# Kernel optimization log

Hardware: AMD Instinct MI355X
Metric: run time of the kernel (lower is better)

## Reference

```python
import jax, jax.numpy as jnp
import numpy as np

B, S, Lb, C, CP, H = 64, 4, 64, 32, 16, 4
LN_EPS = 1e-5


def layer_norm(x, g, b):
    mu = jnp.mean(x, axis=-1, keepdims=True)
    var = jnp.mean(jnp.square(x - mu), axis=-1, keepdims=True)
    return (x - mu) * jax.lax.rsqrt(var + LN_EPS) * g + b


def mha(x, w_in, b_in, w_out, b_out, h):
    # torch nn.MultiheadAttention, batch_first, self-attention
    Bx, L, Cx = x.shape
    d = Cx // h
    qkv = x @ w_in.T + b_in                      # (Bx, L, 3C)
    q, k, v = jnp.split(qkv, 3, axis=-1)
    sp = lambda t: t.reshape(Bx, L, h, d).transpose(0, 2, 1, 3)  # (Bx,h,L,d)
    q, k, v = sp(q), sp(k), sp(v)
    scale = 1.0 / jnp.sqrt(jnp.asarray(d, x.dtype))
    attn = jax.nn.softmax(jnp.einsum('bhid,bhjd->bhij', q, k) * scale, axis=-1)
    o = jnp.einsum('bhij,bhjd->bhid', attn, v).transpose(0, 2, 1, 3).reshape(Bx, L, Cx)
    return o @ w_out.T + b_out


def setup_inputs() -> dict:
    key = jax.random.key(0)
    ks = jax.random.split(key, 20)
    g = lambda i, shape, s=0.05: (jax.random.normal(ks[i], shape, dtype=jnp.float32) * s)
    inp = {
        'chip_ctcf': jax.random.normal(ks[0], (B, Lb), dtype=jnp.float32),
        'chip_hac':  jax.random.normal(ks[1], (B, Lb), dtype=jnp.float32),
        'chip_me1':  jax.random.normal(ks[2], (B, Lb), dtype=jnp.float32),
        'chip_me3':  jax.random.normal(ks[3], (B, Lb), dtype=jnp.float32),
        'embed_w': g(4, (C, 1)), 'embed_b': g(5, (C,)),
        'pos_embed': g(6, (1, 1, Lb, C), 0.02),
        'row_in_w': g(7, (3 * C, C)), 'row_in_b': g(8, (3 * C,)),
        'row_out_w': g(9, (C, C)), 'row_out_b': g(10, (C,)),
        'row_ln_g': jnp.ones((C,), jnp.float32), 'row_ln_b': jnp.zeros((C,), jnp.float32),
        'col_in_w': g(11, (3 * C, C)), 'col_in_b': g(12, (3 * C,)),
        'col_out_w': g(13, (C, C)), 'col_out_b': g(14, (C,)),
        'col_ln_g': jnp.ones((C,), jnp.float32), 'col_ln_b': jnp.zeros((C,), jnp.float32),
        'proj_w': g(15, (CP, C * C)), 'proj_b': g(16, (CP,)),
        'pln_g': jnp.ones((CP,), jnp.float32), 'pln_b': jnp.zeros((CP,), jnp.float32),
    }
    return inp


def reference(chip_ctcf, chip_hac, chip_me1, chip_me3,
              embed_w, embed_b, pos_embed,
              row_in_w, row_in_b, row_out_w, row_out_b, row_ln_g, row_ln_b,
              col_in_w, col_in_b, col_out_w, col_out_b, col_ln_g, col_ln_b,
              proj_w, proj_b, pln_g, pln_b):
    Bv = chip_ctcf.shape[0]
    signals = jnp.stack([chip_ctcf, chip_hac, chip_me1, chip_me3], axis=1)  # (B,4,64)
    # Linear(1, C): scalar embed
    msa = signals[..., None] * embed_w[:, 0] + embed_b                      # (B,4,64,C)
    msa = msa + pos_embed
    # row attention over the 64 bins, per track
    x = msa.reshape(Bv * S, Lb, C)
    x = layer_norm(x + mha(x, row_in_w, row_in_b, row_out_w, row_out_b, H), row_ln_g, row_ln_b)
    msa = x.reshape(Bv, S, Lb, C)
    # column attention over the 4 tracks, per bin
    x = msa.transpose(0, 2, 1, 3).reshape(Bv * Lb, S, C)
    x = layer_norm(x + mha(x, col_in_w, col_in_b, col_out_w, col_out_b, H), col_ln_g, col_ln_b)
    msa = x.reshape(Bv, Lb, S, C).transpose(0, 2, 1, 3)                     # (B,4,64,C)
    # outer product of the track-mean (as written in the torch source)
    m = jnp.mean(msa, axis=1)                                               # (B,64,C)
    pair = jnp.einsum('bic,bjd->bijcd', m, m).reshape(Bv, Lb, Lb, C * C)    # (B,64,64,1024)
    nrm = jnp.sqrt(jnp.sum(jnp.square(pair), axis=-1, keepdims=True))
    pair = pair / jnp.maximum(nrm, 1e-6)                                    # F.normalize eps=1e-6
    feat = pair @ proj_w.T + proj_b                                         # (B,64,64,CP)
    feat = layer_norm(feat, pln_g, pln_b)
    feat = feat * jax.nn.sigmoid(feat)                                      # SiLU
    return feat.transpose(0, 3, 1, 2)                                       # (B,CP,64,64)
```

## Files before the change

kernel.cpp:

```cpp
#include <hip/hip_runtime.h>
#include <hip/hip_bf16.h>

#define LN_EPS 1e-5f

__device__ __forceinline__ float dot8(float4 a0, float4 a1, float4 b0, float4 b1) {
    return a0.x * b0.x + a0.y * b0.y + a0.z * b0.z + a0.w * b0.w +
           a1.x * b1.x + a1.y * b1.y + a1.z * b1.z + a1.w * b1.w;
}

__global__ __launch_bounds__(256) void k_row(
    const float* __restrict__ ctcf, const float* __restrict__ hac,
    const float* __restrict__ me1,  const float* __restrict__ me3,
    const float* __restrict__ ew,   const float* __restrict__ eb,
    const float* __restrict__ pe,
    const float* __restrict__ w_in, const float* __restrict__ b_in,
    const float* __restrict__ w_out,const float* __restrict__ b_out,
    const float* __restrict__ ln_g, const float* __restrict__ ln_b,
    float* __restrict__ msaR)
{
    __shared__ float sx[64][33];
    __shared__ float sqkv[64 * 100];
    __shared__ float so[64][33];
    __shared__ float smean[64], srstd[64];

    const int blk = blockIdx.x;
    const int s   = blk & 3;
    const int b   = blk >> 2;
    const int tid = threadIdx.x;

    const float* chip = (s == 0) ? ctcf : (s == 1) ? hac : (s == 2) ? me1 : me3;

    for (int n = tid; n < 2048; n += 256) {
        int l = n >> 5, c = n & 31;
        sx[l][c] = chip[b * 64 + l] * ew[c] + eb[c] + pe[l * 32 + c];
    }
    __syncthreads();

    const int l  = tid & 63;
    const int cg = tid >> 6;

    float xr[32];
#pragma unroll
    for (int c = 0; c < 32; ++c) xr[c] = sx[l][c];

#pragma unroll
    for (int i = 0; i < 24; ++i) {
        int cc = i * 4 + cg;
        const float4* wr4 = (const float4*)&w_in[cc * 32];
        float acc = b_in[cc];
#pragma unroll
        for (int c4 = 0; c4 < 8; ++c4) {
            float4 wv = wr4[c4];
            acc += xr[c4 * 4 + 0] * wv.x + xr[c4 * 4 + 1] * wv.y +
                   xr[c4 * 4 + 2] * wv.z + xr[c4 * 4 + 3] * wv.w;
        }
        sqkv[l * 100 + cc] = acc;
    }
    __syncthreads();

    {
        const int h = cg;
        const float4* qp = (const float4*)&sqkv[l * 100 + h * 8];
        float4 q0 = qp[0], q1 = qp[1];
        const float scale = 0.35355339059327373f;
        float mrun = -1e30f, denom = 0.f, a[8];
#pragma unroll
        for (int dd = 0; dd < 8; ++dd) a[dd] = 0.f;
        for (int j = 0; j < 64; ++j) {
            const float4* kp = (const float4*)&sqkv[j * 100 + 32 + h * 8];
            float4 k0 = kp[0], k1 = kp[1];
            float sc = dot8(q0, q1, k0, k1) * scale;
            const float4* vp = (const float4*)&sqkv[j * 100 + 64 + h * 8];
            float4 v0 = vp[0], v1 = vp[1];
            float mnew = fmaxf(mrun, sc);
            float corr = __expf(mrun - mnew);
            float w = __expf(sc - mnew);
            denom = denom * corr + w;
            a[0] = a[0] * corr + w * v0.x;  a[1] = a[1] * corr + w * v0.y;
            a[2] = a[2] * corr + w * v0.z;  a[3] = a[3] * corr + w * v0.w;
            a[4] = a[4] * corr + w * v1.x;  a[5] = a[5] * corr + w * v1.y;
            a[6] = a[6] * corr + w * v1.z;  a[7] = a[7] * corr + w * v1.w;
            mrun = mnew;
        }
        float inv = 1.f / denom;
#pragma unroll
        for (int dd = 0; dd < 8; ++dd) so[l][h * 8 + dd] = a[dd] * inv;
    }
    __syncthreads();

    {
        float orow[32];
#pragma unroll
        for (int k = 0; k < 32; ++k) orow[k] = so[l][k];
#pragma unroll
        for (int i = 0; i < 8; ++i) {
            int c = i * 4 + cg;
            const float4* wr4 = (const float4*)&w_out[c * 32];
            float acc = b_out[c] + xr[c];
#pragma unroll
            for (int k4 = 0; k4 < 8; ++k4) {
                float4 wv = wr4[k4];
                acc += orow[k4 * 4 + 0] * wv.x + orow[k4 * 4 + 1] * wv.y +
                       orow[k4 * 4 + 2] * wv.z + orow[k4 * 4 + 3] * wv.w;
            }
            sqkv[l * 100 + c] = acc;
        }
    }
    __syncthreads();

    if (tid < 64) {
        float mu = 0.f;
#pragma unroll
        for (int c = 0; c < 32; ++c) mu += sqkv[tid * 100 + c];
        mu *= (1.f / 32.f);
        float var = 0.f;
#pragma unroll
        for (int c = 0; c < 32; ++c) { float d = sqkv[tid * 100 + c] - mu; var += d * d; }
        var *= (1.f / 32.f);
        smean[tid] = mu;
        srstd[tid] = rsqrtf(var + LN_EPS);
    }
    __syncthreads();

    float* outp = msaR + blk * 2048;
    for (int n = tid; n < 2048; n += 256) {
        int ll = n >> 5, c = n & 31;
        outp[n] = (sqkv[ll * 100 + c] - smean[ll]) * srstd[ll] * ln_g[c] + ln_b[c];
    }
}

__global__ __launch_bounds__(256) void k_col(
    const float* __restrict__ msaR,
    const float* __restrict__ w_in, const float* __restrict__ b_in,
    const float* __restrict__ w_out,const float* __restrict__ b_out,
    const float* __restrict__ ln_g, const float* __restrict__ ln_b,
    float* __restrict__ m_out, float* __restrict__ nrm_out)
{
    __shared__ float sx[64][33];
    __shared__ float sqkv[64 * 100];
    __shared__ float so[64][33];
    __shared__ float smean2[64], srstd2[64];
    __shared__ float smv[16][33];

    const int bx = blockIdx.x;
    const int b  = bx >> 2;
    const int l0 = (bx & 3) * 16;
    const int tid = threadIdx.x;

    for (int n = tid; n < 2048; n += 256) {
        int s = n >> 9, lo = (n >> 5) & 15, c = n & 31;
        sx[s * 16 + lo][c] = msaR[((b * 4 + s) * 64 + l0 + lo) * 32 + c];
    }
    __syncthreads();

    const int r  = tid & 63;
    const int sS = r & 3, lo = r >> 2;
    const int cg = tid >> 6;

    float xr[32];
#pragma unroll
    for (int c = 0; c < 32; ++c) xr[c] = sx[sS * 16 + lo][c];

#pragma unroll
    for (int i = 0; i < 24; ++i) {
        int cc = i * 4 + cg;
        const float4* wr4 = (const float4*)&w_in[cc * 32];
        float acc = b_in[cc];
#pragma unroll
        for (int c4 = 0; c4 < 8; ++c4) {
            float4 wv = wr4[c4];
            acc += xr[c4 * 4 + 0] * wv.x + xr[c4 * 4 + 1] * wv.y +
                   xr[c4 * 4 + 2] * wv.z + xr[c4 * 4 + 3] * wv.w;
        }
        sqkv[r * 100 + cc] = acc;
    }
    __syncthreads();

    {
        const int la = tid >> 4, h = (tid >> 2) & 3, ia = tid & 3;
        const float scale = 0.35355339059327373f;
        const float4* qp = (const float4*)&sqkv[(la * 4 + ia) * 100 + h * 8];
        float4 q0 = qp[0], q1 = qp[1];
        float sc[4];
        float mx = -1e30f;
#pragma unroll
        for (int jj = 0; jj < 4; ++jj) {
            const float4* kp = (const float4*)&sqkv[(la * 4 + jj) * 100 + 32 + h * 8];
            sc[jj] = dot8(q0, q1, kp[0], kp[1]) * scale;
            mx = fmaxf(mx, sc[jj]);
        }
        float den = 0.f;
#pragma unroll
        for (int jj = 0; jj < 4; ++jj) { sc[jj] = __expf(sc[jj] - mx); den += sc[jj]; }
        float inv = 1.f / den;
        float a[8];
#pragma unroll
        for (int dd = 0; dd < 8; ++dd) a[dd] = 0.f;
#pragma unroll
        for (int jj = 0; jj < 4; ++jj) {
            const float4* vp = (const float4*)&sqkv[(la * 4 + jj) * 100 + 64 + h * 8];
            float4 v0 = vp[0], v1 = vp[1];
            float wgt = sc[jj];
            a[0] += wgt * v0.x;  a[1] += wgt * v0.y;
            a[2] += wgt * v0.z;  a[3] += wgt * v0.w;
            a[4] += wgt * v1.x;  a[5] += wgt * v1.y;
            a[6] += wgt * v1.z;  a[7] += wgt * v1.w;
        }
#pragma unroll
        for (int dd = 0; dd < 8; ++dd) so[la * 4 + ia][h * 8 + dd] = a[dd] * inv;
    }
    __syncthreads();

    {
        float orow[32];
#pragma unroll
        for (int k = 0; k < 32; ++k) orow[k] = so[r][k];
#pragma unroll
        for (int i = 0; i < 8; ++i) {
            int c = i * 4 + cg;
            const float4* wr4 = (const float4*)&w_out[c * 32];
            float acc = b_out[c] + xr[c];
#pragma unroll
            for (int k4 = 0; k4 < 8; ++k4) {
                float4 wv = wr4[k4];
                acc += orow[k4 * 4 + 0] * wv.x + orow[k4 * 4 + 1] * wv.y +
                       orow[k4 * 4 + 2] * wv.z + orow[k4 * 4 + 3] * wv.w;
            }
            sqkv[r * 100 + c] = acc;
        }
    }
    __syncthreads();

    if (tid < 64) {
        float mu = 0.f;
#pragma unroll
        for (int c = 0; c < 32; ++c) mu += sqkv[tid * 100 + c];
        mu *= (1.f / 32.f);
        float var = 0.f;
#pragma unroll
        for (int c = 0; c < 32; ++c) { float d = sqkv[tid * 100 + c] - mu; var += d * d; }
        var *= (1.f / 32.f);
        smean2[tid] = mu;
        srstd2[tid] = rsqrtf(var + LN_EPS);
    }
    __syncthreads();

    for (int pass = 0; pass < 2; ++pass) {
        int idx = pass * 256 + tid;
        int loo = idx >> 5, c = idx & 31;
        float acc = 0.f;
#pragma unroll
        for (int ss = 0; ss < 4; ++ss) {
            int rr = loo * 4 + ss;
            acc += (sqkv[rr * 100 + c] - smean2[rr]) * srstd2[rr];
        }
        float mval = 0.25f * acc * ln_g[c] + ln_b[c];
        m_out[(b * 64 + l0 + loo) * 32 + c] = mval;
        smv[loo][c] = mval * mval;
    }
    __syncthreads();

    if (tid < 16) {
        float sum = 0.f;
#pragma unroll
        for (int c = 0; c < 32; ++c) sum += smv[tid][c];
        nrm_out[b * 64 + l0 + tid] = sqrtf(sum);
    }
}

__global__ __launch_bounds__(256) void k_pair(
    const float* __restrict__ m, const float* __restrict__ nrm,
    const float* __restrict__ pw, const float* __restrict__ pb,
    const float* __restrict__ pg, const float* __restrict__ pbeta,
    float* __restrict__ out)
{
    __shared__ float smj[64][36];
    __shared__ float sT[8 * 520];
    __shared__ float snj[64];
    __shared__ float sbias[16], sgam[16], sbet[16];

    const int bx = blockIdx.x;
    const int b  = bx >> 3;
    const int i0 = (bx & 7) * 8;
    const int tid = threadIdx.x;
    const int lane = tid & 63, w = tid >> 6;

    const int rem0 = lane + 128 * w;
    const int rem1 = rem0 + 64;
    const float* pw0 = pw + (rem0 >> 5) * 1024 + (rem0 & 31);
    const float* pw1 = pw + (rem1 >> 5) * 1024 + (rem1 & 31);
    float w0[32], w1[32];
#pragma unroll
    for (int c = 0; c < 32; ++c) { w0[c] = pw0[c * 32]; w1[c] = pw1[c * 32]; }

    const float* mb = m + b * 2048;
    for (int n = tid; n < 2048; n += 256) smj[n >> 5][n & 31] = mb[n];
    if (tid < 64) snj[tid] = nrm[b * 64 + tid];
    if (tid < 16) {
        sbias[tid] = pb[tid];
        sgam[tid]  = pg[tid];
        sbet[tid]  = pbeta[tid];
    }
    __syncthreads();

#pragma unroll
    for (int il = 0; il < 8; ++il) {
        const float4* mr4 = (const float4*)&smj[i0 + il][0];
        float a0 = 0.f, a1 = 0.f;
#pragma unroll
        for (int c4 = 0; c4 < 8; ++c4) {
            float4 mv = mr4[c4];
            a0 += mv.x * w0[c4 * 4 + 0] + mv.y * w0[c4 * 4 + 1] +
                  mv.z * w0[c4 * 4 + 2] + mv.w * w0[c4 * 4 + 3];
            a1 += mv.x * w1[c4 * 4 + 0] + mv.y * w1[c4 * 4 + 1] +
                  mv.z * w1[c4 * 4 + 2] + mv.w * w1[c4 * 4 + 3];
        }
        sT[il * 520 + rem0] = a0;
        sT[il * 520 + rem1] = a1;
    }
    __syncthreads();

    const int j = lane;
    float mj[32];
    {
        const float4* mjp = (const float4*)&smj[j][0];
#pragma unroll
        for (int d4 = 0; d4 < 8; ++d4) {
            float4 t = mjp[d4];
            mj[d4 * 4 + 0] = t.x;  mj[d4 * 4 + 1] = t.y;
            mj[d4 * 4 + 2] = t.z;  mj[d4 * 4 + 3] = t.w;
        }
    }
    const float nj = snj[j];

#pragma unroll
    for (int q = 0; q < 2; ++q) {
        const int il = w * 2 + q;
        const int ig = i0 + il;
        const float invn = 1.f / fmaxf(snj[ig] * nj, 1e-6f);
        float f[16];
#pragma unroll
        for (int cp = 0; cp < 16; ++cp) {
            const float4* tr = (const float4*)&sT[il * 520 + cp * 32];
            float acc = 0.f;
#pragma unroll
            for (int d4 = 0; d4 < 8; ++d4) {
                float4 tv = tr[d4];
                acc += tv.x * mj[d4 * 4 + 0] + tv.y * mj[d4 * 4 + 1] +
                       tv.z * mj[d4 * 4 + 2] + tv.w * mj[d4 * 4 + 3];
            }
            f[cp] = acc * invn + sbias[cp];
        }
        float mu = 0.f;
#pragma unroll
        for (int cp = 0; cp < 16; ++cp) mu += f[cp];
        mu *= (1.f / 16.f);
        float var = 0.f;
#pragma unroll
        for (int cp = 0; cp < 16; ++cp) { float d = f[cp] - mu; var += d * d; }
        var *= (1.f / 16.f);
        const float rstd = rsqrtf(var + LN_EPS);
#pragma unroll
        for (int cp = 0; cp < 16; ++cp) {
            float v = (f[cp] - mu) * rstd * sgam[cp] + sbet[cp];
            float sl = v / (1.f + __expf(-v));
            out[((b * 16 + cp) * 64 + ig) * 64 + j] = sl;
        }
    }
}

extern "C" void kernel_launch(void* const* d_in, const int* in_sizes, int n_in,
                              void* d_out, int out_size, void* d_ws, size_t ws_size,
                              hipStream_t stream) {
    const float* ctcf  = (const float*)d_in[0];
    const float* hac   = (const float*)d_in[1];
    const float* me1   = (const float*)d_in[2];
    const float* me3   = (const float*)d_in[3];
    const float* ew    = (const float*)d_in[4];
    const float* ebias = (const float*)d_in[5];
    const float* pe    = (const float*)d_in[6];
    const float* riw   = (const float*)d_in[7];
    const float* rib   = (const float*)d_in[8];
    const float* row_  = (const float*)d_in[9];
    const float* rob   = (const float*)d_in[10];
    const float* rlg   = (const float*)d_in[11];
    const float* rlb   = (const float*)d_in[12];
    const float* ciw   = (const float*)d_in[13];
    const float* cib   = (const float*)d_in[14];
    const float* cow   = (const float*)d_in[15];
    const float* cob   = (const float*)d_in[16];
    const float* clg   = (const float*)d_in[17];
    const float* clb   = (const float*)d_in[18];
    const float* pw    = (const float*)d_in[19];
    const float* pb    = (const float*)d_in[20];
    const float* pg    = (const float*)d_in[21];
    const float* pbt   = (const float*)d_in[22];

    float* out = (float*)d_out;

    float* msaR = (float*)d_out;
    float* mbuf = (float*)d_ws;
    float* nbuf = mbuf + 64 * 64 * 32;

    k_row<<<256, 256, 0, stream>>>(ctcf, hac, me1, me3, ew, ebias, pe,
                                   riw, rib, row_, rob, rlg, rlb, msaR);
    k_col<<<256, 256, 0, stream>>>(msaR, ciw, cib, cow, cob, clg, clb,
                                   mbuf, nbuf);
    k_pair<<<512, 256, 0, stream>>>(mbuf, nbuf, pw, pb, pg, pbt, out);
}
```

Baseline: 156.4 us.

## Widen blocks across all three kernels and split row attention keys across lanes

Raises k_row and k_col to 1024 threads and k_pair to 512 threads per block, so each thread computes fewer projection outputs and k_pair holds one weight column instead of two. In row attention, each query is now handled by four lanes that each scan a quarter of the keys, and their online-softmax states are merged with xor shuffles. The goal is to cut per-thread serial work and register pressure and raise parallelism on a small 256-block grid. In exchange it adds shuffle and exp overhead, leaves idle threads in the col attention and reduction phases, and re-reads the residual from shared memory.

```diff
diff --git a/kernel.cpp b/kernel.cpp
--- a/kernel.cpp
+++ b/kernel.cpp
@@ -1,5 +1,4 @@
 #include <hip/hip_runtime.h>
-#include <hip/hip_bf16.h>
 
 #define LN_EPS 1e-5f
 
@@ -8,7 +7,7 @@
            a1.x * b1.x + a1.y * b1.y + a1.z * b1.z + a1.w * b1.w;
 }
 
-__global__ __launch_bounds__(256) void k_row(
+__global__ __launch_bounds__(1024) void k_row(
     const float* __restrict__ ctcf, const float* __restrict__ hac,
     const float* __restrict__ me1,  const float* __restrict__ me3,
     const float* __restrict__ ew,   const float* __restrict__ eb,
@@ -30,7 +29,7 @@
 
     const float* chip = (s == 0) ? ctcf : (s == 1) ? hac : (s == 2) ? me1 : me3;
 
-    for (int n = tid; n < 2048; n += 256) {
+    for (int n = tid; n < 2048; n += 1024) {
         int l = n >> 5, c = n & 31;
         sx[l][c] = chip[b * 64 + l] * ew[c] + eb[c] + pe[l * 32 + c];
     }
@@ -39,37 +38,41 @@
     const int l  = tid & 63;
     const int cg = tid >> 6;
 
-    float xr[32];
-#pragma unroll
-    for (int c = 0; c < 32; ++c) xr[c] = sx[l][c];
-
-#pragma unroll
-    for (int i = 0; i < 24; ++i) {
-        int cc = i * 4 + cg;
-        const float4* wr4 = (const float4*)&w_in[cc * 32];
-        float acc = b_in[cc];
-#pragma unroll
-        for (int c4 = 0; c4 < 8; ++c4) {
-            float4 wv = wr4[c4];
-            acc += xr[c4 * 4 + 0] * wv.x + xr[c4 * 4 + 1] * wv.y +
-                   xr[c4 * 4 + 2] * wv.z + xr[c4 * 4 + 3] * wv.w;
-        }
-        sqkv[l * 100 + cc] = acc;
-    }
-    __syncthreads();
-
-    {
-        const int h = cg;
-        const float4* qp = (const float4*)&sqkv[l * 100 + h * 8];
+    {
+        float xr[32];
+#pragma unroll
+        for (int c = 0; c < 32; ++c) xr[c] = sx[l][c];
+#pragma unroll
+        for (int i = 0; i < 6; ++i) {
+            int cc = i * 16 + cg;
+            const float4* wr4 = (const float4*)&w_in[cc * 32];
+            float acc = b_in[cc];
+#pragma unroll
+            for (int c4 = 0; c4 < 8; ++c4) {
+                float4 wv = wr4[c4];
+                acc += xr[c4 * 4 + 0] * wv.x + xr[c4 * 4 + 1] * wv.y +
+                       xr[c4 * 4 + 2] * wv.z + xr[c4 * 4 + 3] * wv.w;
+            }
+            sqkv[l * 100 + cc] = acc;
+        }
+    }
+    __syncthreads();
+
+    {
+        const int h  = tid >> 8;
+        const int la = (tid >> 2) & 63;
+        const int kc = tid & 3;
+        const float4* qp = (const float4*)&sqkv[la * 100 + h * 8];
         float4 q0 = qp[0], q1 = qp[1];
         const float scale = 0.35355339059327373f;
         float mrun = -1e30f, denom = 0.f, a[8];
 #pragma unroll
         for (int dd = 0; dd < 8; ++dd) a[dd] = 0.f;
-        for (int j = 0; j < 64; ++j) {
+#pragma unroll
+        for (int jj = 0; jj < 16; ++jj) {
+            const int j = kc * 16 + jj;
             const float4* kp = (const float4*)&sqkv[j * 100 + 32 + h * 8];
-            float4 k0 = kp[0], k1 = kp[1];
-            float sc = dot8(q0, q1, k0, k1) * scale;
+            float sc = dot8(q0, q1, kp[0], kp[1]) * scale;
             const float4* vp = (const float4*)&sqkv[j * 100 + 64 + h * 8];
             float4 v0 = vp[0], v1 = vp[1];
             float mnew = fmaxf(mrun, sc);
@@ -82,9 +85,29 @@
             a[6] = a[6] * corr + w * v1.z;  a[7] = a[7] * corr + w * v1.w;
             mrun = mnew;
         }
+#pragma unroll
+        for (int off = 1; off <= 2; off <<= 1) {
+            float mo = __shfl_xor(mrun, off, 64);
+            float dn = __shfl_xor(denom, off, 64);
+            float mn = fmaxf(mrun, mo);
+            float c1 = __expf(mrun - mn);
+            float c2 = __expf(mo - mn);
+            denom = denom * c1 + dn * c2;
+#pragma unroll
+            for (int dd = 0; dd < 8; ++dd) {
+                float ao = __shfl_xor(a[dd], off, 64);
+                a[dd] = a[dd] * c1 + ao * c2;
+            }
+            mrun = mn;
+        }
         float inv = 1.f / denom;
-#pragma unroll
-        for (int dd = 0; dd < 8; ++dd) so[l][h * 8 + dd] = a[dd] * inv;
+        float r0, r1;
+        if      (kc == 0) { r0 = a[0]; r1 = a[1]; }
+        else if (kc == 1) { r0 = a[2]; r1 = a[3]; }
+        else if (kc == 2) { r0 = a[4]; r1 = a[5]; }
+        else              { r0 = a[6]; r1 = a[7]; }
+        so[la][h * 8 + kc * 2 + 0] = r0 * inv;
+        so[la][h * 8 + kc * 2 + 1] = r1 * inv;
     }
     __syncthreads();
 
@@ -93,10 +116,10 @@
 #pragma unroll
         for (int k = 0; k < 32; ++k) orow[k] = so[l][k];
 #pragma unroll
-        for (int i = 0; i < 8; ++i) {
-            int c = i * 4 + cg;
+        for (int i = 0; i < 2; ++i) {
+            int c = i * 16 + cg;
             const float4* wr4 = (const float4*)&w_out[c * 32];
-            float acc = b_out[c] + xr[c];
+            float acc = b_out[c] + sx[l][c];
 #pragma unroll
             for (int k4 = 0; k4 < 8; ++k4) {
                 float4 wv = wr4[k4];
@@ -123,13 +146,13 @@
     __syncthreads();
 
     float* outp = msaR + blk * 2048;
-    for (int n = tid; n < 2048; n += 256) {
+    for (int n = tid; n < 2048; n += 1024) {
         int ll = n >> 5, c = n & 31;
         outp[n] = (sqkv[ll * 100 + c] - smean[ll]) * srstd[ll] * ln_g[c] + ln_b[c];
     }
 }
 
-__global__ __launch_bounds__(256) void k_col(
+__global__ __launch_bounds__(1024) void k_col(
     const float* __restrict__ msaR,
     const float* __restrict__ w_in, const float* __restrict__ b_in,
     const float* __restrict__ w_out,const float* __restrict__ b_out,
@@ -147,7 +170,7 @@
     const int l0 = (bx & 3) * 16;
     const int tid = threadIdx.x;
 
-    for (int n = tid; n < 2048; n += 256) {
+    for (int n = tid; n < 2048; n += 1024) {
         int s = n >> 9, lo = (n >> 5) & 15, c = n & 31;
         sx[s * 16 + lo][c] = msaR[((b * 4 + s) * 64 + l0 + lo) * 32 + c];
     }
@@ -157,26 +180,27 @@
     const int sS = r & 3, lo = r >> 2;
     const int cg = tid >> 6;
 
-    float xr[32];
-#pragma unroll
-    for (int c = 0; c < 32; ++c) xr[c] = sx[sS * 16 + lo][c];
-
-#pragma unroll
-    for (int i = 0; i < 24; ++i) {
-        int cc = i * 4 + cg;
-        const float4* wr4 = (const float4*)&w_in[cc * 32];
-        float acc = b_in[cc];
-#pragma unroll
-        for (int c4 = 0; c4 < 8; ++c4) {
-            float4 wv = wr4[c4];
-            acc += xr[c4 * 4 + 0] * wv.x + xr[c4 * 4 + 1] * wv.y +
-                   xr[c4 * 4 + 2] * wv.z + xr[c4 * 4 + 3] * wv.w;
-        }
-        sqkv[r * 100 + cc] = acc;
-    }
-    __syncthreads();
-
-    {
+    {
+        float xr[32];
+#pragma unroll
+        for (int c = 0; c < 32; ++c) xr[c] = sx[sS * 16 + lo][c];
+#pragma unroll
+        for (int i = 0; i < 6; ++i) {
+            int cc = i * 16 + cg;
+            const float4* wr4 = (const float4*)&w_in[cc * 32];
+            float acc = b_in[cc];
+#pragma unroll
+            for (int c4 = 0; c4 < 8; ++c4) {
+                float4 wv = wr4[c4];
+                acc += xr[c4 * 4 + 0] * wv.x + xr[c4 * 4 + 1] * wv.y +
+                       xr[c4 * 4 + 2] * wv.z + xr[c4 * 4 + 3] * wv.w;
+            }
+            sqkv[r * 100 + cc] = acc;
+        }
+    }
+    __syncthreads();
+
+    if (tid < 256) {
         const int la = tid >> 4, h = (tid >> 2) & 3, ia = tid & 3;
         const float scale = 0.35355339059327373f;
         const float4* qp = (const float4*)&sqkv[(la * 4 + ia) * 100 + h * 8];
@@ -216,10 +240,10 @@
 #pragma unroll
         for (int k = 0; k < 32; ++k) orow[k] = so[r][k];
 #pragma unroll
-        for (int i = 0; i < 8; ++i) {
-            int c = i * 4 + cg;
+        for (int i = 0; i < 2; ++i) {
+            int c = i * 16 + cg;
             const float4* wr4 = (const float4*)&w_out[c * 32];
-            float acc = b_out[c] + xr[c];
+            float acc = b_out[c] + sx[sS * 16 + lo][c];
 #pragma unroll
             for (int k4 = 0; k4 < 8; ++k4) {
                 float4 wv = wr4[k4];
@@ -245,9 +269,8 @@
     }
     __syncthreads();
 
-    for (int pass = 0; pass < 2; ++pass) {
-        int idx = pass * 256 + tid;
-        int loo = idx >> 5, c = idx & 31;
+    if (tid < 512) {
+        int loo = tid >> 5, c = tid & 31;
         float acc = 0.f;
 #pragma unroll
         for (int ss = 0; ss < 4; ++ss) {
@@ -268,7 +291,7 @@
     }
 }
 
-__global__ __launch_bounds__(256) void k_pair(
+__global__ __launch_bounds__(512, 4) void k_pair(
     const float* __restrict__ m, const float* __restrict__ nrm,
     const float* __restrict__ pw, const float* __restrict__ pb,
     const float* __restrict__ pg, const float* __restrict__ pbeta,
@@ -285,16 +308,14 @@
     const int tid = threadIdx.x;
     const int lane = tid & 63, w = tid >> 6;
 
-    const int rem0 = lane + 128 * w;
-    const int rem1 = rem0 + 64;
-    const float* pw0 = pw + (rem0 >> 5) * 1024 + (rem0 & 31);
-    const float* pw1 = pw + (rem1 >> 5) * 1024 + (rem1 & 31);
-    float w0[32], w1[32];
-#pragma unroll
-    for (int c = 0; c < 32; ++c) { w0[c] = pw0[c * 32]; w1[c] = pw1[c * 32]; }
+    const int rem = tid;
+    const float* pwp = pw + (rem >> 5) * 1024 + (rem & 31);
+    float w0[32];
+#pragma unroll
+    for (int c = 0; c < 32; ++c) w0[c] = pwp[c * 32];
 
     const float* mb = m + b * 2048;
-    for (int n = tid; n < 2048; n += 256) smj[n >> 5][n & 31] = mb[n];
+    for (int n = tid; n < 2048; n += 512) smj[n >> 5][n & 31] = mb[n];
     if (tid < 64) snj[tid] = nrm[b * 64 + tid];
     if (tid < 16) {
         sbias[tid] = pb[tid];
@@ -306,17 +327,14 @@
 #pragma unroll
     for (int il = 0; il < 8; ++il) {
         const float4* mr4 = (const float4*)&smj[i0 + il][0];
-        float a0 = 0.f, a1 = 0.f;
+        float a0 = 0.f;
 #pragma unroll
         for (int c4 = 0; c4 < 8; ++c4) {
             float4 mv = mr4[c4];
             a0 += mv.x * w0[c4 * 4 + 0] + mv.y * w0[c4 * 4 + 1] +
                   mv.z * w0[c4 * 4 + 2] + mv.w * w0[c4 * 4 + 3];
-            a1 += mv.x * w1[c4 * 4 + 0] + mv.y * w1[c4 * 4 + 1] +
-                  mv.z * w1[c4 * 4 + 2] + mv.w * w1[c4 * 4 + 3];
-        }
-        sT[il * 520 + rem0] = a0;
-        sT[il * 520 + rem1] = a1;
+        }
+        sT[il * 520 + rem] = a0;
     }
     __syncthreads();
 
@@ -333,9 +351,8 @@
     }
     const float nj = snj[j];
 
-#pragma unroll
-    for (int q = 0; q < 2; ++q) {
-        const int il = w * 2 + q;
+    {
+        const int il = w;
         const int ig = i0 + il;
         const float invn = 1.f / fmaxf(snj[ig] * nj, 1e-6f);
         float f[16];
@@ -402,9 +419,9 @@
     float* mbuf = (float*)d_ws;
     float* nbuf = mbuf + 64 * 64 * 32;
 
-    k_row<<<256, 256, 0, stream>>>(ctcf, hac, me1, me3, ew, ebias, pe,
-                                   riw, rib, row_, rob, rlg, rlb, msaR);
-    k_col<<<256, 256, 0, stream>>>(msaR, ciw, cib, cow, cob, clg, clb,
-                                   mbuf, nbuf);
-    k_pair<<<512, 256, 0, stream>>>(mbuf, nbuf, pw, pb, pg, pbt, out);
+    k_row<<<256, 1024, 0, stream>>>(ctcf, hac, me1, me3, ew, ebias, pe,
+                                    riw, rib, row_, rob, rlg, rlb, msaR);
+    k_col<<<256, 1024, 0, stream>>>(msaR, ciw, cib, cow, cob, clg, clb,
+                                    mbuf, nbuf);
+    k_pair<<<512, 512, 0, stream>>>(mbuf, nbuf, pw, pb, pg, pbt, out);
 }
```

New measurement: 149.2 us. 1.05x faster.
